# Kernel optimization log

Measured on AMD Instinct MI355X. Metric: run time of the kernel, lower is better.

Reference implementation:

```python
import jax, jax.numpy as jnp
import numpy as np

HIDDEN = 256
TOPK = 16
SINK_BLOCKS = 5
TAU = 1.0
SOFT_ALPHA = 8.0
LN_EPS = 1e-5


def setup_inputs() -> dict:
    key = jax.random.key(0)
    ks = jax.random.split(key, 8)
    B, T, QD, KD, J = 2, 1024, 1024, 1024, 64
    H = HIDDEN
    H3 = 3 * H
    s = 0.02
    return {
        "Q": jax.random.normal(ks[0], (B, T, QD), dtype=jnp.float32),
        "K": jax.random.normal(ks[1], (B, J, KD), dtype=jnp.float32),
        "Wq": jax.random.normal(ks[2], (H, QD), dtype=jnp.float32) * s,
        "Wk": jax.random.normal(ks[3], (H, KD), dtype=jnp.float32) * s,
        "ln_g": jnp.ones((H3,), dtype=jnp.float32),
        "ln_b": jnp.zeros((H3,), dtype=jnp.float32),
        "Wu": jax.random.normal(ks[4], (H, H3), dtype=jnp.float32) * s,
        "bu": jnp.zeros((H,), dtype=jnp.float32),
        "Wv": jax.random.normal(ks[5], (H, H3), dtype=jnp.float32) * s,
        "bv": jnp.zeros((H,), dtype=jnp.float32),
        "Wo": jax.random.normal(ks[6], (1, H), dtype=jnp.float32) * s,
        "bo": jnp.zeros((1,), dtype=jnp.float32),
        "chunk_len": 16,
        "L_ctx": 1024,
    }


def _forward(Q, K, Wq, Wk, ln_g, ln_b, Wu, bu, Wv, bv, Wo, bo, chunk_len, L_ctx):
    B, T, _ = Q.shape
    J = K.shape[1]
    # ---- GatedScorer ----
    q = jnp.einsum('btd,hd->bth', Q, Wq)  # (B,T,H)
    k = jnp.einsum('bjd,hd->bjh', K, Wk)  # (B,J,H)
    H = q.shape[-1]
    qb = jnp.broadcast_to(q[:, :, None, :], (B, T, J, H))
    kb = jnp.broadcast_to(k[:, None, :, :], (B, T, J, H))
    x = jnp.concatenate([qb, kb, qb * kb], axis=-1)  # (B,T,J,3H)
    mu = jnp.mean(x, axis=-1, keepdims=True)
    var = jnp.mean((x - mu) ** 2, axis=-1, keepdims=True)
    x = (x - mu) / jnp.sqrt(var + LN_EPS) * ln_g + ln_b
    U = jnp.einsum('btjc,hc->btjh', x, Wu) + bu
    V = jnp.einsum('btjc,hc->btjh', x, Wv) + bv
    Z = U * jax.nn.gelu(V, approximate=False)
    logits = jnp.einsum('btjh,oh->btjo', Z, Wo)[..., 0] + bo[0]  # (B,T,J)

    # ---- top-k chunk selection (deterministic path, use_learnable_k=False) ----
    sink = int(min(max(0, SINK_BLOCKS), J))
    J_tail = J - sink
    topk_main = max(min(J, TOPK) - sink, 0)
    logits_tail = logits[..., sink:]  # (B,T,J_tail)
    causal = jnp.arange(J_tail)[None, :] <= jnp.arange(T)[:, None]  # tril(T,J_tail)
    masked = jnp.where(causal[None], logits_tail, -jnp.inf)
    _, idx_tail = jax.lax.top_k(masked, topk_main)
    idx_tail = idx_tail + sink
    sink_idx = jnp.broadcast_to(jnp.arange(sink)[None, None, :], (B, T, sink))
    idx = jnp.concatenate([sink_idx, idx_tail], axis=-1)  # (B,T,sink+topk_main)

    # ---- soft warmup weights ----
    w_soft = jax.nn.softmax(logits / TAU, axis=-1)  # (B,T,J)

    # ---- build_block_bias_from_topk ----
    num_chunks = (L_ctx + chunk_len - 1) // chunk_len
    sel = jnp.zeros((B, T, num_chunks), dtype=bool)
    sel = sel.at[jnp.arange(B)[:, None, None], jnp.arange(T)[None, :, None], idx].set(True)
    token_chunk = jnp.clip(jnp.arange(L_ctx) // chunk_len, 0, num_chunks - 1)  # (L_ctx,)
    sel_tok = jnp.take(sel, token_chunk, axis=-1)  # (B,T,L_ctx)
    per_chunk_bias = -SOFT_ALPHA * (1.0 - w_soft)  # (B,T,J)
    bias = jnp.take(per_chunk_bias, token_chunk, axis=-1)  # (B,T,L_ctx)
    bias = jnp.where(sel_tok, 0.0, bias)
    tri = jnp.arange(L_ctx)[None, :] > jnp.arange(T)[:, None]  # triu(T,L_ctx, diag=1)
    bias = jnp.where(tri[None], -jnp.inf, bias)
    return logits, bias


def reference(Q, K, Wq, Wk, ln_g, ln_b, Wu, bu, Wv, bv, Wo, bo, chunk_len, L_ctx):
    return _forward(Q, K, Wq, Wk, ln_g, ln_b, Wu, bu, Wv, bv, Wo, bo, chunk_len, L_ctx)
```

## Files before the change

### kernel.cpp

```cpp
#include <hip/hip_runtime.h>
#include <hip/hip_bf16.h>
#include <math.h>

#define H3 768

#define OFF_Q     0u
#define OFF_K     524288u
#define OFF_UVK   557056u
#define OFF_SQ    622592u
#define OFF_SQ2   624768u
#define OFF_WGU   626944u
#define OFF_WGV   627200u
#define OFF_CU    627456u
#define OFF_CV    627712u

#define BO_UVQ   0u
#define BO_WQF   1048576u
#define BO_WKF   1310720u
#define BO_BPK   1572864u
#define BO_WQBF  1703936u
#define BO_WKBF  1835008u

typedef __attribute__((ext_vector_type(8))) short bf16x8;
typedef __attribute__((ext_vector_type(4))) float f32x4;

__device__ __forceinline__ float bf2f(short s) {
    return __uint_as_float(((unsigned)(unsigned short)s) << 16);
}
union bfu { __hip_bfloat162 h; short2 s; };
__device__ __forceinline__ void split2(float a, float b, short* hi2, short* lo2) {
    bfu h; h.h = __float22bfloat162_rn(float2{a, b});
    float fa = bf2f(h.s.x), fb = bf2f(h.s.y);
    bfu l; l.h = __float22bfloat162_rn(float2{a - fa, b - fb});
    hi2[0] = h.s.x; hi2[1] = h.s.y;
    lo2[0] = l.s.x; lo2[1] = l.s.y;
}
__device__ __forceinline__ void split8(const float* v, bf16x8* vh, bf16x8* vl) {
    short h2[2], l2[2];
#pragma unroll
    for (int i = 0; i < 4; i++) {
        split2(v[2 * i], v[2 * i + 1], h2, l2);
        (*vh)[2 * i] = h2[0]; (*vh)[2 * i + 1] = h2[1];
        (*vl)[2 * i] = l2[0]; (*vl)[2 * i + 1] = l2[1];
    }
}

__device__ __forceinline__ float gelu_fast(float v) {
    float ar = v * 0.70710678118654752440f;
    float a = fabsf(ar);
    float t = __builtin_amdgcn_rcpf(fmaf(0.3275911f, a, 1.0f));
    float p = fmaf(fmaf(fmaf(fmaf(1.061405429f, t, -1.453152027f), t,
                             1.421413741f), t, -0.284496736f), t, 0.254829592f) * t;
    float e = __expf(-ar * ar);
    float er = fmaf(-p, e, 1.0f);
    er = copysignf(er, ar);
    return 0.5f * v * (1.0f + er);
}

__device__ __forceinline__ float wave_reduce_add(float v) {
#pragma unroll
    for (int off = 32; off > 0; off >>= 1) v += __shfl_xor(v, off, 64);
    return v;
}

__global__ __launch_bounds__(256) void prep(const float* __restrict__ Wq,
                                            const float* __restrict__ Wk,
                                            const float* __restrict__ Wu,
                                            const float* __restrict__ Wv,
                                            const float* __restrict__ g,
                                            const float* __restrict__ lb,
                                            const float* __restrict__ bu,
                                            const float* __restrict__ bv,
                                            float* __restrict__ ws,
                                            float* __restrict__ bsc) {
    int tid = threadIdx.x;
    int bid = blockIdx.x;
    if (bid >= 512) {
        ws[(bid - 512) * 256 + tid] = 0.0f;
        return;
    }
    if (bid < 64) {
        int h = bid * 4 + (tid >> 6);
        int lane = tid & 63;
        float su = 0.f, sv = 0.f, tu = 0.f, tv = 0.f;
#pragma unroll
        for (int i = 0; i < 12; i++) {
            int c = lane + 64 * i;
            float gg = g[c], bb = lb[c];
            float wu = Wu[h * H3 + c], wv = Wv[h * H3 + c];
            su += wu * gg; sv += wv * gg; tu += wu * bb; tv += wv * bb;
        }
        su = wave_reduce_add(su); sv = wave_reduce_add(sv);
        tu = wave_reduce_add(tu); tv = wave_reduce_add(tv);
        if (lane == 0) {
            ws[OFF_WGU + h] = su; ws[OFF_WGV + h] = sv;
            ws[OFF_CU + h] = tu + bu[h]; ws[OFF_CV + h] = tv + bv[h];
        }
        return;
    }
    float v8[8];
    bf16x8 vh, vl;
    if (bid < 320) {
        const float* W; bf16x8* dst;
        int idx;
        if (bid < 192) { idx = (bid - 64) * 256 + tid; W = Wq; dst = (bf16x8*)(bsc + BO_WQF); }
        else { idx = (bid - 192) * 256 + tid; W = Wk; dst = (bf16x8*)(bsc + BO_WKF); }
        int n = idx >> 7, k8 = idx & 127;
        const float* src = W + (size_t)n * 1024 + k8 * 8;
        *(float4*)&v8[0] = *(const float4*)src;
        *(float4*)&v8[4] = *(const float4*)(src + 4);
        split8(v8, &vh, &vl);
        int kc = k8 >> 2, grp = k8 & 3, lane = grp * 16 + (n & 15), ntg = n >> 4;
        size_t s0 = ((size_t)(kc * 16 + ntg) * 2) * 64 + lane;
        dst[s0] = vh; dst[s0 + 64] = vl;
        return;
    }
    int idx, c0;
    bf16x8* dst;
    int n;
    if (bid < 384) {
        idx = (bid - 320) * 256 + tid;
        n = idx >> 5; c0 = (idx & 31) * 8;
        dst = (bf16x8*)(bsc + BO_WQBF);
    } else if (bid < 448) {
        idx = (bid - 384) * 256 + tid;
        n = idx >> 5; c0 = 256 + (idx & 31) * 8;
        dst = (bf16x8*)(bsc + BO_WKBF);
    } else {
        idx = (bid - 448) * 256 + tid;
        n = idx >> 5; c0 = 512 + (idx & 31) * 8;
        dst = (bf16x8*)(bsc + BO_BPK);
    }
    int h, uv;
    if (bid < 448) { uv = (n < 256) ? 0 : 1; h = (n < 256) ? n : n - 256; }
    else {
        int ntg0 = n >> 4, cc = n & 15;
        uv = ntg0 & 1;
        h = ((ntg0 >> 3) << 6) | (((ntg0 >> 1) & 3) << 4) | cc;
    }
    const float* W = uv ? Wv : Wu;
#pragma unroll
    for (int i = 0; i < 8; i++) v8[i] = W[(size_t)h * H3 + c0 + i] * g[c0 + i];
    split8(v8, &vh, &vl);
    int k8 = (c0 & 255) >> 3;
    int kc = k8 >> 2, grp = k8 & 3, lane = grp * 16 + (n & 15), ntg = n >> 4;
    size_t s0 = ((size_t)(kc * 32 + ntg) * 2) * 64 + lane;
    dst[s0] = vh; dst[s0 + 64] = vl;
}

__global__ __launch_bounds__(256) void proj_mfma(const float* __restrict__ Q,
                                                 const float* __restrict__ Kin,
                                                 const float* __restrict__ bsc,
                                                 float* __restrict__ ws) {
    __shared__ __align__(16) short Ah[2][32 * 40], Al[2][32 * 40];
    int tid = threadIdx.x, bx = blockIdx.x, by = blockIdx.y, ks = blockIdx.z;
    const float* A; float* C; const bf16x8* BF;
    if (by < 64) {
        A = Q + (size_t)by * 32 * 1024;
        C = ws + OFF_Q + (size_t)by * 32 * 256;
        BF = (const bf16x8*)(bsc + BO_WQF);
    } else {
        A = Kin + (size_t)(by - 64) * 32 * 1024;
        C = ws + OFF_K + (size_t)(by - 64) * 32 * 256;
        BF = (const bf16x8*)(bsc + BO_WKF);
    }
    int w = tid >> 6, l = tid & 63, c15 = l & 15, grp = l >> 4;
    int mt = w & 1, np = w >> 1;
    int srow = tid >> 3, scol = (tid & 7) * 4;
    const float* arow = A + (size_t)srow * 1024 + ks * 512 + scol;
    f32x4 acc[2];
    acc[0] = (f32x4){0.f, 0.f, 0.f, 0.f};
    acc[1] = (f32x4){0.f, 0.f, 0.f, 0.f};
    float4 a4 = *(const float4*)&arow[0];
    for (int kc = 0; kc < 16; kc++) {
        int pb = kc & 1;
        short h4[4], l4[4];
        split2(a4.x, a4.y, &h4[0], &l4[0]);
        split2(a4.z, a4.w, &h4[2], &l4[2]);
        int ao = srow * 40 + scol;
        *(short4*)&Ah[pb][ao] = *(short4*)&h4[0];
        *(short4*)&Al[pb][ao] = *(short4*)&l4[0];
        if (kc < 15) a4 = *(const float4*)&arow[(kc + 1) * 32];
        __syncthreads();
        int fo = (mt * 16 + c15) * 40 + grp * 8;
        bf16x8 afh = *(const bf16x8*)&Ah[pb][fo];
        bf16x8 afl = *(const bf16x8*)&Al[pb][fo];
        int kcg = ks * 16 + kc;
        bf16x8 bh[2], bl[2];
#pragma unroll
        for (int i = 0; i < 2; i++) {
            int ntg = bx * 4 + 2 * np + i;
            size_t fi = ((size_t)(kcg * 16 + ntg) * 2) * 64 + l;
            bh[i] = BF[fi]; bl[i] = BF[fi + 64];
        }
#pragma unroll
        for (int i = 0; i < 2; i++)
            acc[i] = __builtin_amdgcn_mfma_f32_16x16x32_bf16(afl, bh[i], acc[i], 0, 0, 0);
#pragma unroll
        for (int i = 0; i < 2; i++)
            acc[i] = __builtin_amdgcn_mfma_f32_16x16x32_bf16(afh, bl[i], acc[i], 0, 0, 0);
#pragma unroll
        for (int i = 0; i < 2; i++)
            acc[i] = __builtin_amdgcn_mfma_f32_16x16x32_bf16(afh, bh[i], acc[i], 0, 0, 0);
    }
#pragma unroll
    for (int r = 0; r < 4; r++) {
        int rloc = mt * 16 + grp * 4 + r;
#pragma unroll
        for (int i = 0; i < 2; i++)
            atomicAdd(&C[(size_t)rloc * 256 + bx * 64 + (2 * np + i) * 16 + c15], acc[i][r]);
    }
}

__global__ __launch_bounds__(256) void uv_mfma(float* __restrict__ ws,
                                               float* __restrict__ bsc) {
    __shared__ __align__(16) short Ah[32 * 40], Al[32 * 40];
    int tid = threadIdx.x, bx = blockIdx.x, by = blockIdx.y;
    const float* A; float* C; const bf16x8* BF; int sbase;
    if (by < 64) {
        A = ws + OFF_Q + (size_t)by * 32 * 256;
        C = bsc + BO_UVQ + (size_t)by * 32 * 512;
        BF = (const bf16x8*)(bsc + BO_WQBF);
        sbase = by * 32;
    } else {
        A = ws + OFF_K + (size_t)(by - 64) * 32 * 256;
        C = ws + OFF_UVK + (size_t)(by - 64) * 32 * 512;
        BF = (const bf16x8*)(bsc + BO_WKBF);
        sbase = 2048 + (by - 64) * 32;
    }
    int w = tid >> 6, l = tid & 63, c15 = l & 15, grp = l >> 4;
    int mt = w & 1, np = w >> 1;
    int srow = tid >> 3, scol = (tid & 7) * 4;
    f32x4 acc[2];
    acc[0] = (f32x4){0.f, 0.f, 0.f, 0.f};
    acc[1] = (f32x4){0.f, 0.f, 0.f, 0.f};
    float s1 = 0.f, s2 = 0.f;
    for (int kc = 0; kc < 8; kc++) {
        float4 a4 = *(const float4*)&A[(size_t)srow * 256 + kc * 32 + scol];
        if (bx == 0) {
            s1 += (a4.x + a4.y) + (a4.z + a4.w);
            s2 = fmaf(a4.x, a4.x, s2); s2 = fmaf(a4.y, a4.y, s2);
            s2 = fmaf(a4.z, a4.z, s2); s2 = fmaf(a4.w, a4.w, s2);
        }
        short h4v[4], l4v[4];
        split2(a4.x, a4.y, &h4v[0], &l4v[0]);
        split2(a4.z, a4.w, &h4v[2], &l4v[2]);
        int ao = srow * 40 + scol;
        *(short4*)&Ah[ao] = *(short4*)&h4v[0];
        *(short4*)&Al[ao] = *(short4*)&l4v[0];
        __syncthreads();
        int fo = (mt * 16 + c15) * 40 + grp * 8;
        bf16x8 afh = *(const bf16x8*)&Ah[fo];
        bf16x8 afl = *(const bf16x8*)&Al[fo];
        bf16x8 bh[2], bl[2];
#pragma unroll
        for (int i = 0; i < 2; i++) {
            int ntg = bx * 4 + np * 2 + i;
            size_t fi = ((size_t)(kc * 32 + ntg) * 2) * 64 + l;
            bh[i] = BF[fi]; bl[i] = BF[fi + 64];
        }
#pragma unroll
        for (int i = 0; i < 2; i++)
            acc[i] = __builtin_amdgcn_mfma_f32_16x16x32_bf16(afl, bh[i], acc[i], 0, 0, 0);
#pragma unroll
        for (int i = 0; i < 2; i++)
            acc[i] = __builtin_amdgcn_mfma_f32_16x16x32_bf16(afh, bl[i], acc[i], 0, 0, 0);
#pragma unroll
        for (int i = 0; i < 2; i++)
            acc[i] = __builtin_amdgcn_mfma_f32_16x16x32_bf16(afh, bh[i], acc[i], 0, 0, 0);
        __syncthreads();
    }
    if (bx == 0) {
        s1 += __shfl_xor(s1, 1, 64); s1 += __shfl_xor(s1, 2, 64); s1 += __shfl_xor(s1, 4, 64);
        s2 += __shfl_xor(s2, 1, 64); s2 += __shfl_xor(s2, 2, 64); s2 += __shfl_xor(s2, 4, 64);
        if ((tid & 7) == 0) {
            ws[OFF_SQ + sbase + srow] = s1;
            ws[OFF_SQ2 + sbase + srow] = s2;
        }
    }
#pragma unroll
    for (int i = 0; i < 2; i++)
#pragma unroll
        for (int r = 0; r < 4; r++)
            C[(size_t)(mt * 16 + grp * 4 + r) * 512 + bx * 64 + np * 32 + i * 16 + c15] = acc[i][r];
}

__global__ __launch_bounds__(256, 2) void main_mfma(const float* __restrict__ ws,
                                                    const float* __restrict__ bsc,
                                                    const float* __restrict__ Wo,
                                                    const float* __restrict__ bo,
                                                    float* __restrict__ logits) {
    __shared__ float kk[256];
    __shared__ __align__(16) short Ah[8][64 * 32];
    __shared__ __align__(16) short Al[8][64 * 32];
    __shared__ float mu_s[64], inv_s[64];
    __shared__ float part_s[4][64];
    int tid = threadIdx.x;
    int bidf = blockIdx.x;
    int ti = ((bidf & 7) << 1) | ((bidf >> 3) & 1);
    int j = (bidf >> 4) & 63;
    int b = bidf >> 10;
    int t0 = ti << 6;
    int bj = (b << 6) | j;
    int rot8 = bidf & 7;
    kk[tid] = ws[OFF_K + bj * 256 + tid];
    int w = tid >> 6, l = tid & 63, c15 = l & 15, grp = l >> 4;
    int srow = tid >> 2, scol = (tid & 3) * 8;
    const float* qrow = ws + OFF_Q + (size_t)((b << 10) + t0 + srow) * 256 + scol;
    const bf16x8* bpk = (const bf16x8*)(bsc + BO_BPK);
    const float* UVQ = bsc + BO_UVQ;
    int ntg0 = w * 8;
    float wgu_r[4], wgv_r[4], cu_r[4], cv_r[4], wo_r[4], uk_r[4], vk_r[4];
    int h4[4];
#pragma unroll
    for (int a = 0; a < 4; a++) {
        int h = (w << 6) | (a << 4) | c15;
        h4[a] = h;
        wgu_r[a] = ws[OFF_WGU + h]; wgv_r[a] = ws[OFF_WGV + h];
        cu_r[a] = ws[OFF_CU + h]; cv_r[a] = ws[OFF_CV + h];
        wo_r[a] = Wo[h];
        uk_r[a] = ws[OFF_UVK + (size_t)bj * 512 + h];
        vk_r[a] = ws[OFF_UVK + (size_t)bj * 512 + 256 + h];
    }
    f32x4 acc[4][8];
#pragma unroll
    for (int mt = 0; mt < 4; mt++) {
#pragma unroll
        for (int r4 = 0; r4 < 4; r4++) {
            int row = (b << 10) + t0 + mt * 16 + grp * 4 + r4;
            const float* uvq = UVQ + (size_t)row * 512;
#pragma unroll
            for (int a = 0; a < 4; a++) {
                acc[mt][2 * a][r4]     = uvq[h4[a]] + uk_r[a];
                acc[mt][2 * a + 1][r4] = uvq[256 + h4[a]] + vk_r[a];
            }
        }
    }
    float s1 = 0.f, s2 = 0.f;
    int ao = ((((srow >> 4) << 6) | ((tid & 3) << 4) | (srow & 15)) << 3);
    __syncthreads();
#pragma unroll
    for (int kc = 0; kc < 8; kc++) {
        float q8[8], kv[8];
        *(float4*)&q8[0] = *(const float4*)&qrow[kc * 32];
        *(float4*)&q8[4] = *(const float4*)&qrow[kc * 32 + 4];
        *(float4*)&kv[0] = *(const float4*)&kk[kc * 32 + scol];
        *(float4*)&kv[4] = *(const float4*)&kk[kc * 32 + scol + 4];
        bf16x8 vh, vl;
        short htmp[2], ltmp[2];
#pragma unroll
        for (int i = 0; i < 4; i++) {
            float a = q8[2 * i] * kv[2 * i];
            float c = q8[2 * i + 1] * kv[2 * i + 1];
            s1 += a + c;
            s2 = fmaf(a, a, s2); s2 = fmaf(c, c, s2);
            split2(a, c, htmp, ltmp);
            vh[2 * i] = htmp[0]; vh[2 * i + 1] = htmp[1];
            vl[2 * i] = ltmp[0]; vl[2 * i + 1] = ltmp[1];
        }
        *(bf16x8*)&Ah[kc][ao] = vh;
        *(bf16x8*)&Al[kc][ao] = vl;
    }
    s1 += __shfl_xor(s1, 1, 64); s1 += __shfl_xor(s1, 2, 64);
    s2 += __shfl_xor(s2, 1, 64); s2 += __shfl_xor(s2, 2, 64);
    if ((tid & 3) == 0) {
        int row = (b << 10) + t0 + srow;
        float sq = s1 + ws[OFF_SQ + row] + ws[OFF_SQ + 2048 + bj];
        float sq2 = s2 + ws[OFF_SQ2 + row] + ws[OFF_SQ2 + 2048 + bj];
        float muv = sq * (1.0f / 768.0f);
        float ex2 = sq2 * (1.0f / 768.0f);
        mu_s[srow] = muv;
        inv_s[srow] = 1.0f / sqrtf(ex2 - muv * muv + 1e-5f);
    }
    __syncthreads();
#pragma unroll
    for (int ii = 0; ii < 8; ii++) {
        int kcg = (ii + rot8) & 7;
        bf16x8 afh[4], afl[4];
#pragma unroll
        for (int mt = 0; mt < 4; mt++) {
            int fo = ((mt << 6) | l) << 3;
            afh[mt] = *(const bf16x8*)&Ah[kcg][fo];
            afl[mt] = *(const bf16x8*)&Al[kcg][fo];
        }
        const bf16x8* bpc = bpk + ((size_t)(kcg * 32 + ntg0) * 2) * 64 + l;
#pragma unroll
        for (int nt = 0; nt < 8; nt++) {
            bf16x8 bh = bpc[(size_t)nt * 128];
            bf16x8 bl = bpc[(size_t)nt * 128 + 64];
#pragma unroll
            for (int mt = 0; mt < 4; mt++)
                acc[mt][nt] = __builtin_amdgcn_mfma_f32_16x16x32_bf16(afl[mt], bh, acc[mt][nt], 0, 0, 0);
#pragma unroll
            for (int mt = 0; mt < 4; mt++)
                acc[mt][nt] = __builtin_amdgcn_mfma_f32_16x16x32_bf16(afh[mt], bl, acc[mt][nt], 0, 0, 0);
#pragma unroll
            for (int mt = 0; mt < 4; mt++)
                acc[mt][nt] = __builtin_amdgcn_mfma_f32_16x16x32_bf16(afh[mt], bh, acc[mt][nt], 0, 0, 0);
        }
    }
#pragma unroll
    for (int mt = 0; mt < 4; mt++) {
#pragma unroll
        for (int r4 = 0; r4 < 4; r4++) {
            int r = mt * 16 + grp * 4 + r4;
            float muv = mu_s[r], invv = inv_s[r];
            float part = 0.f;
#pragma unroll
            for (int a = 0; a < 4; a++) {
                float U = fmaf(invv, fmaf(-muv, wgu_r[a], acc[mt][2 * a][r4]), cu_r[a]);
                float V = fmaf(invv, fmaf(-muv, wgv_r[a], acc[mt][2 * a + 1][r4]), cv_r[a]);
                part = fmaf(wo_r[a] * U, gelu_fast(V), part);
            }
            part += __shfl_xor(part, 1, 64);
            part += __shfl_xor(part, 2, 64);
            part += __shfl_xor(part, 4, 64);
            part += __shfl_xor(part, 8, 64);
            if (c15 == 0) part_s[w][r] = part;
        }
    }
    __syncthreads();
    if (tid < 64) {
        float v = bo[0] + part_s[0][tid] + part_s[1][tid] + part_s[2][tid] + part_s[3][tid];
        logits[(size_t)((b << 10) + t0 + tid) * 64 + j] = v;
    }
}

__global__ __launch_bounds__(256) void topk_bias(const float* __restrict__ logits,
                                                 float* __restrict__ bias,
                                                 const int* __restrict__ p_cl,
                                                 const int* __restrict__ p_L) {
    int wv = threadIdx.x >> 6, lane = threadIdx.x & 63;
    int row = blockIdx.x * 4 + wv;
    int t = row & 1023;
    __shared__ float pcb[4][64];
    float L = logits[(size_t)row * 64 + lane];
    float mx = L;
#pragma unroll
    for (int off = 32; off > 0; off >>= 1) mx = fmaxf(mx, __shfl_xor(mx, off, 64));
    float e = expf(L - mx);
    float s = wave_reduce_add(e);
    pcb[wv][lane] = -8.0f * (1.0f - e / s);
    bool valid = (lane >= 5) && ((lane - 5) <= t);
    float val = (lane >= 5) ? (valid ? L : -INFINITY) : -INFINITY;
    int idv = (lane >= 5) ? lane : (1 << 28);
    unsigned long long selmask = 0x1Full;
    for (int it = 0; it < 11; it++) {
        float bv = val; int bi = idv;
#pragma unroll
        for (int off = 32; off > 0; off >>= 1) {
            float ov = __shfl_xor(bv, off, 64);
            int oi = __shfl_xor(bi, off, 64);
            if (ov > bv || (ov == bv && oi < bi)) { bv = ov; bi = oi; }
        }
        selmask |= 1ull << bi;
        if (lane == bi) { val = -INFINITY; idv = (1 << 27); }
    }
    int clen = p_cl[0], Lctx = p_L[0];
    int nch1 = (Lctx + clen - 1) / clen - 1;
    bool p2 = (clen & (clen - 1)) == 0;
    int sh = 31 - __clz(clen);
    float* brow = bias + (size_t)row * Lctx;
    if ((Lctx & 3) == 0) {
        float4* brow4 = (float4*)brow;
        for (int q = lane; q < (Lctx >> 2); q += 64) {
            float o[4];
#pragma unroll
            for (int i = 0; i < 4; i++) {
                int ll = 4 * q + i;
                unsigned cq = p2 ? ((unsigned)ll >> sh) : ((unsigned)ll / (unsigned)clen);
                int c = min(min(cq, (unsigned)nch1), 63u);
                float v;
                if (ll > t) v = -1e30f;
                else if ((selmask >> c) & 1ull) v = 0.0f;
                else v = pcb[wv][c];
                o[i] = v;
            }
            brow4[q] = *(float4*)&o[0];
        }
    } else {
        for (int ll = lane; ll < Lctx; ll += 64) {
            unsigned cq = p2 ? ((unsigned)ll >> sh) : ((unsigned)ll / (unsigned)clen);
            int c = min(min(cq, (unsigned)nch1), 63u);
            float v;
            if (ll > t) v = -1e30f;
            else if ((selmask >> c) & 1ull) v = 0.0f;
            else v = pcb[wv][c];
            brow[ll] = v;
        }
    }
}

extern "C" void kernel_launch(void* const* d_in, const int* in_sizes, int n_in,
                              void* d_out, int out_size, void* d_ws, size_t ws_size,
                              hipStream_t stream) {
    const float* Q   = (const float*)d_in[0];
    const float* Kin = (const float*)d_in[1];
    const float* Wq  = (const float*)d_in[2];
    const float* Wk  = (const float*)d_in[3];
    const float* g   = (const float*)d_in[4];
    const float* lb  = (const float*)d_in[5];
    const float* Wu  = (const float*)d_in[6];
    const float* bu  = (const float*)d_in[7];
    const float* Wv  = (const float*)d_in[8];
    const float* bv  = (const float*)d_in[9];
    const float* Wo  = (const float*)d_in[10];
    const float* bo  = (const float*)d_in[11];
    const int* p_cl  = (const int*)d_in[12];
    const int* p_L   = (const int*)d_in[13];
    float* ws = (float*)d_ws;
    float* logits = (float*)d_out;
    float* bias = (float*)d_out + (size_t)2 * 1024 * 64;

    prep<<<2688, 256, 0, stream>>>(Wq, Wk, Wu, Wv, g, lb, bu, bv, ws, bias);
    proj_mfma<<<dim3(4, 68, 2), 256, 0, stream>>>(Q, Kin, bias, ws);
    uv_mfma<<<dim3(8, 68), 256, 0, stream>>>(ws, bias);
    main_mfma<<<2048, 256, 0, stream>>>(ws, bias, Wo, bo, logits);
    topk_bias<<<512, 256, 0, stream>>>(logits, bias, p_cl, p_L);
}
```

Before: 224.4 us.

## Switch main GEMM from 16x16x32 to 32x32x16 MFMA with matching layouts

The main fused LayerNorm/GEMM kernel now uses 32x32x16 bf16 MFMA tiles (two 32-row M tiles by four 32-column N tiles per wave) in place of 16x16x32 tiles. The weight-packing kernel and the LDS A-fragment layout are rewritten to match the new operand layout, and the epilogue row mapping and cross-lane reduction are adapted. Larger MFMA tiles cut LDS and global fragment loads per FLOP and reduce instruction count. The trade-off is different register pressure and changed LDS access patterns, which may cause bank conflicts.

```diff
diff --git a/kernel.cpp b/kernel.cpp
--- a/kernel.cpp
+++ b/kernel.cpp
@@ -23,6 +23,7 @@
 
 typedef __attribute__((ext_vector_type(8))) short bf16x8;
 typedef __attribute__((ext_vector_type(4))) float f32x4;
+typedef __attribute__((ext_vector_type(16))) float f32x16;
 
 __device__ __forceinline__ float bf2f(short s) {
     return __uint_as_float(((unsigned)(unsigned short)s) << 16);
@@ -115,37 +116,50 @@
         dst[s0] = vh; dst[s0 + 64] = vl;
         return;
     }
-    int idx, c0;
-    bf16x8* dst;
-    int n;
-    if (bid < 384) {
-        idx = (bid - 320) * 256 + tid;
-        n = idx >> 5; c0 = (idx & 31) * 8;
-        dst = (bf16x8*)(bsc + BO_WQBF);
-    } else if (bid < 448) {
-        idx = (bid - 384) * 256 + tid;
-        n = idx >> 5; c0 = 256 + (idx & 31) * 8;
-        dst = (bf16x8*)(bsc + BO_WKBF);
-    } else {
-        idx = (bid - 448) * 256 + tid;
-        n = idx >> 5; c0 = 512 + (idx & 31) * 8;
-        dst = (bf16x8*)(bsc + BO_BPK);
-    }
-    int h, uv;
-    if (bid < 448) { uv = (n < 256) ? 0 : 1; h = (n < 256) ? n : n - 256; }
-    else {
-        int ntg0 = n >> 4, cc = n & 15;
-        uv = ntg0 & 1;
-        h = ((ntg0 >> 3) << 6) | (((ntg0 >> 1) & 3) << 4) | cc;
-    }
-    const float* W = uv ? Wv : Wu;
-#pragma unroll
-    for (int i = 0; i < 8; i++) v8[i] = W[(size_t)h * H3 + c0 + i] * g[c0 + i];
-    split8(v8, &vh, &vl);
-    int k8 = (c0 & 255) >> 3;
-    int kc = k8 >> 2, grp = k8 & 3, lane = grp * 16 + (n & 15), ntg = n >> 4;
-    size_t s0 = ((size_t)(kc * 32 + ntg) * 2) * 64 + lane;
-    dst[s0] = vh; dst[s0 + 64] = vl;
+    if (bid < 448) {
+        int idx, c0;
+        bf16x8* dst;
+        if (bid < 384) {
+            idx = (bid - 320) * 256 + tid;
+            c0 = (idx & 31) * 8;
+            dst = (bf16x8*)(bsc + BO_WQBF);
+        } else {
+            idx = (bid - 384) * 256 + tid;
+            c0 = 256 + (idx & 31) * 8;
+            dst = (bf16x8*)(bsc + BO_WKBF);
+        }
+        int n = idx >> 5;
+        int uv = (n < 256) ? 0 : 1;
+        int h = (n < 256) ? n : n - 256;
+        const float* W = uv ? Wv : Wu;
+#pragma unroll
+        for (int i = 0; i < 8; i++) v8[i] = W[(size_t)h * H3 + c0 + i] * g[c0 + i];
+        split8(v8, &vh, &vl);
+        int k8 = (c0 & 255) >> 3;
+        int kc = k8 >> 2, grp = k8 & 3, lane = grp * 16 + (n & 15), ntg = n >> 4;
+        size_t s0 = ((size_t)(kc * 32 + ntg) * 2) * 64 + lane;
+        dst[s0] = vh; dst[s0 + 64] = vl;
+        return;
+    }
+    {
+        int idx = (bid - 448) * 256 + tid;
+        int n = idx >> 5;
+        int c0 = 512 + (idx & 31) * 8;
+        int T = n >> 5, c31 = n & 31;
+        int wq = T >> 2, tt = T & 3;
+        int uv = tt >> 1;
+        int h = wq * 64 + (tt & 1) * 32 + c31;
+        const float* W = uv ? Wv : Wu;
+#pragma unroll
+        for (int i = 0; i < 8; i++) v8[i] = W[(size_t)h * H3 + c0 + i] * g[c0 + i];
+        split8(v8, &vh, &vl);
+        bf16x8* dst = (bf16x8*)(bsc + BO_BPK);
+        int k8 = (c0 & 255) >> 3;
+        int ks = k8 >> 1, kg = k8 & 1;
+        int lane = kg * 32 + c31;
+        size_t s0 = ((size_t)(ks * 16 + T) * 2) * 64 + lane;
+        dst[s0] = vh; dst[s0 + 64] = vl;
+    }
 }
 
 __global__ __launch_bounds__(256) void proj_mfma(const float* __restrict__ Q,
@@ -291,8 +305,8 @@
                                                     const float* __restrict__ bo,
                                                     float* __restrict__ logits) {
     __shared__ float kk[256];
-    __shared__ __align__(16) short Ah[8][64 * 32];
-    __shared__ __align__(16) short Al[8][64 * 32];
+    __shared__ __align__(16) short Ah[16384];
+    __shared__ __align__(16) short Al[16384];
     __shared__ float mu_s[64], inv_s[64];
     __shared__ float part_s[4][64];
     int tid = threadIdx.x;
@@ -304,40 +318,39 @@
     int bj = (b << 6) | j;
     int rot8 = bidf & 7;
     kk[tid] = ws[OFF_K + bj * 256 + tid];
-    int w = tid >> 6, l = tid & 63, c15 = l & 15, grp = l >> 4;
+    int w = tid >> 6, l = tid & 63, c31 = l & 31, half32 = l >> 5;
     int srow = tid >> 2, scol = (tid & 3) * 8;
     const float* qrow = ws + OFF_Q + (size_t)((b << 10) + t0 + srow) * 256 + scol;
     const bf16x8* bpk = (const bf16x8*)(bsc + BO_BPK);
     const float* UVQ = bsc + BO_UVQ;
-    int ntg0 = w * 8;
-    float wgu_r[4], wgv_r[4], cu_r[4], cv_r[4], wo_r[4], uk_r[4], vk_r[4];
-    int h4[4];
-#pragma unroll
-    for (int a = 0; a < 4; a++) {
-        int h = (w << 6) | (a << 4) | c15;
-        h4[a] = h;
-        wgu_r[a] = ws[OFF_WGU + h]; wgv_r[a] = ws[OFF_WGV + h];
-        cu_r[a] = ws[OFF_CU + h]; cv_r[a] = ws[OFF_CV + h];
-        wo_r[a] = Wo[h];
-        uk_r[a] = ws[OFF_UVK + (size_t)bj * 512 + h];
-        vk_r[a] = ws[OFF_UVK + (size_t)bj * 512 + 256 + h];
-    }
-    f32x4 acc[4][8];
-#pragma unroll
-    for (int mt = 0; mt < 4; mt++) {
-#pragma unroll
-        for (int r4 = 0; r4 < 4; r4++) {
-            int row = (b << 10) + t0 + mt * 16 + grp * 4 + r4;
+    float wgu_r[2], wgv_r[2], cu_r[2], cv_r[2], wo_r[2], uk_r[2], vk_r[2];
+    int h2c[2];
+#pragma unroll
+    for (int tch = 0; tch < 2; tch++) {
+        int h = (w << 6) | (tch << 5) | c31;
+        h2c[tch] = h;
+        wgu_r[tch] = ws[OFF_WGU + h]; wgv_r[tch] = ws[OFF_WGV + h];
+        cu_r[tch] = ws[OFF_CU + h]; cv_r[tch] = ws[OFF_CV + h];
+        wo_r[tch] = Wo[h];
+        uk_r[tch] = ws[OFF_UVK + (size_t)bj * 512 + h];
+        vk_r[tch] = ws[OFF_UVK + (size_t)bj * 512 + 256 + h];
+    }
+    f32x16 acc[2][4];
+#pragma unroll
+    for (int mt2 = 0; mt2 < 2; mt2++) {
+#pragma unroll
+        for (int reg = 0; reg < 16; reg++) {
+            int row = (b << 10) + t0 + mt2 * 32 + (reg & 3) + 8 * (reg >> 2) + 4 * half32;
             const float* uvq = UVQ + (size_t)row * 512;
 #pragma unroll
-            for (int a = 0; a < 4; a++) {
-                acc[mt][2 * a][r4]     = uvq[h4[a]] + uk_r[a];
-                acc[mt][2 * a + 1][r4] = uvq[256 + h4[a]] + vk_r[a];
+            for (int tch = 0; tch < 2; tch++) {
+                acc[mt2][tch][reg]     = uvq[h2c[tch]] + uk_r[tch];
+                acc[mt2][tch + 2][reg] = uvq[256 + h2c[tch]] + vk_r[tch];
             }
         }
     }
     float s1 = 0.f, s2 = 0.f;
-    int ao = ((((srow >> 4) << 6) | ((tid & 3) << 4) | (srow & 15)) << 3);
+    int base = ((((scol >> 4) * 2 + (srow >> 5)) * 64 + ((scol >> 3) & 1) * 32 + (srow & 31)) << 3);
     __syncthreads();
 #pragma unroll
     for (int kc = 0; kc < 8; kc++) {
@@ -358,8 +371,8 @@
             vh[2 * i] = htmp[0]; vh[2 * i + 1] = htmp[1];
             vl[2 * i] = ltmp[0]; vl[2 * i + 1] = ltmp[1];
         }
-        *(bf16x8*)&Ah[kc][ao] = vh;
-        *(bf16x8*)&Al[kc][ao] = vl;
+        *(bf16x8*)&Ah[base + kc * 2048] = vh;
+        *(bf16x8*)&Al[base + kc * 2048] = vl;
     }
     s1 += __shfl_xor(s1, 1, 64); s1 += __shfl_xor(s1, 2, 64);
     s2 += __shfl_xor(s2, 1, 64); s2 += __shfl_xor(s2, 2, 64);
@@ -373,50 +386,52 @@
         inv_s[srow] = 1.0f / sqrtf(ex2 - muv * muv + 1e-5f);
     }
     __syncthreads();
-#pragma unroll
-    for (int ii = 0; ii < 8; ii++) {
-        int kcg = (ii + rot8) & 7;
-        bf16x8 afh[4], afl[4];
-#pragma unroll
-        for (int mt = 0; mt < 4; mt++) {
-            int fo = ((mt << 6) | l) << 3;
-            afh[mt] = *(const bf16x8*)&Ah[kcg][fo];
-            afl[mt] = *(const bf16x8*)&Al[kcg][fo];
-        }
-        const bf16x8* bpc = bpk + ((size_t)(kcg * 32 + ntg0) * 2) * 64 + l;
-#pragma unroll
-        for (int nt = 0; nt < 8; nt++) {
-            bf16x8 bh = bpc[(size_t)nt * 128];
-            bf16x8 bl = bpc[(size_t)nt * 128 + 64];
-#pragma unroll
-            for (int mt = 0; mt < 4; mt++)
-                acc[mt][nt] = __builtin_amdgcn_mfma_f32_16x16x32_bf16(afl[mt], bh, acc[mt][nt], 0, 0, 0);
-#pragma unroll
-            for (int mt = 0; mt < 4; mt++)
-                acc[mt][nt] = __builtin_amdgcn_mfma_f32_16x16x32_bf16(afh[mt], bl, acc[mt][nt], 0, 0, 0);
-#pragma unroll
-            for (int mt = 0; mt < 4; mt++)
-                acc[mt][nt] = __builtin_amdgcn_mfma_f32_16x16x32_bf16(afh[mt], bh, acc[mt][nt], 0, 0, 0);
-        }
-    }
-#pragma unroll
-    for (int mt = 0; mt < 4; mt++) {
-#pragma unroll
-        for (int r4 = 0; r4 < 4; r4++) {
-            int r = mt * 16 + grp * 4 + r4;
-            float muv = mu_s[r], invv = inv_s[r];
+    int rotk = rot8 << 1;
+#pragma unroll
+    for (int ii = 0; ii < 16; ii++) {
+        int ks = (ii + rotk) & 15;
+        bf16x8 afh[2], afl[2];
+#pragma unroll
+        for (int mt2 = 0; mt2 < 2; mt2++) {
+            int fo = ks * 1024 + mt2 * 512 + (l << 3);
+            afh[mt2] = *(const bf16x8*)&Ah[fo];
+            afl[mt2] = *(const bf16x8*)&Al[fo];
+        }
+        const bf16x8* bpc = bpk + (((size_t)(ks * 16 + w * 4)) << 7) + l;
+#pragma unroll
+        for (int T = 0; T < 4; T++) {
+            bf16x8 bh = bpc[(size_t)T * 128];
+            bf16x8 bl = bpc[(size_t)T * 128 + 64];
+#pragma unroll
+            for (int mt2 = 0; mt2 < 2; mt2++)
+                acc[mt2][T] = __builtin_amdgcn_mfma_f32_32x32x16_bf16(afl[mt2], bh, acc[mt2][T], 0, 0, 0);
+#pragma unroll
+            for (int mt2 = 0; mt2 < 2; mt2++)
+                acc[mt2][T] = __builtin_amdgcn_mfma_f32_32x32x16_bf16(afh[mt2], bl, acc[mt2][T], 0, 0, 0);
+#pragma unroll
+            for (int mt2 = 0; mt2 < 2; mt2++)
+                acc[mt2][T] = __builtin_amdgcn_mfma_f32_32x32x16_bf16(afh[mt2], bh, acc[mt2][T], 0, 0, 0);
+        }
+    }
+#pragma unroll
+    for (int mt2 = 0; mt2 < 2; mt2++) {
+#pragma unroll
+        for (int reg = 0; reg < 16; reg++) {
+            int rloc = mt2 * 32 + (reg & 3) + 8 * (reg >> 2) + 4 * half32;
+            float muv = mu_s[rloc], invv = inv_s[rloc];
             float part = 0.f;
 #pragma unroll
-            for (int a = 0; a < 4; a++) {
-                float U = fmaf(invv, fmaf(-muv, wgu_r[a], acc[mt][2 * a][r4]), cu_r[a]);
-                float V = fmaf(invv, fmaf(-muv, wgv_r[a], acc[mt][2 * a + 1][r4]), cv_r[a]);
-                part = fmaf(wo_r[a] * U, gelu_fast(V), part);
+            for (int tch = 0; tch < 2; tch++) {
+                float U = fmaf(invv, fmaf(-muv, wgu_r[tch], acc[mt2][tch][reg]), cu_r[tch]);
+                float V = fmaf(invv, fmaf(-muv, wgv_r[tch], acc[mt2][tch + 2][reg]), cv_r[tch]);
+                part = fmaf(wo_r[tch] * U, gelu_fast(V), part);
             }
             part += __shfl_xor(part, 1, 64);
             part += __shfl_xor(part, 2, 64);
             part += __shfl_xor(part, 4, 64);
             part += __shfl_xor(part, 8, 64);
-            if (c15 == 0) part_s[w][r] = part;
+            part += __shfl_xor(part, 16, 64);
+            if (c31 == 0) part_s[w][rloc] = part;
         }
     }
     __syncthreads();
```

Measured after the change: 252.5 us. 1.13x slower.
